# Kernel tuning notes

Hardware: AMD Instinct MI355X
Metric: run time of the kernel (lower is better)

## Reference

```python
import jax, jax.numpy as jnp
import numpy as np

D_MODEL = 1024
NUM_HEADS = 16
D_K = D_MODEL // NUM_HEADS


def setup_inputs() -> dict:
    key = jax.random.key(0)
    ks = jax.random.split(key, 9)
    B, S = 4, 2048
    s = 1.0 / np.sqrt(D_MODEL)
    inp = {
        "x": jax.random.normal(ks[0], (B, S, D_MODEL), dtype=jnp.float32),
        "wq": jax.random.uniform(ks[1], (D_MODEL, D_MODEL), jnp.float32, -s, s),
        "bq": jax.random.uniform(ks[2], (D_MODEL,), jnp.float32, -s, s),
        "wk": jax.random.uniform(ks[3], (D_MODEL, D_MODEL), jnp.float32, -s, s),
        "bk": jax.random.uniform(ks[4], (D_MODEL,), jnp.float32, -s, s),
        "wv": jax.random.uniform(ks[5], (D_MODEL, D_MODEL), jnp.float32, -s, s),
        "bv": jax.random.uniform(ks[6], (D_MODEL,), jnp.float32, -s, s),
        "wo": jax.random.uniform(ks[7], (D_MODEL, D_MODEL), jnp.float32, -s, s),
        "bo": jax.random.uniform(ks[8], (D_MODEL,), jnp.float32, -s, s),
    }
    return inp


def reference(x, wq, bq, wk, bk, wv, bv, wo, bo):
    B, S, _ = x.shape
    H, Dk = NUM_HEADS, D_K
    # QKV projections; weights stored as (in, out) so y = x @ w + b
    q = (x @ wq + bq).reshape(B, S, H, Dk).transpose(0, 2, 1, 3)  # (B,H,S,Dk)
    k = (x @ wk + bk).reshape(B, S, H, Dk).transpose(0, 2, 1, 3)
    v = (x @ wv + bv).reshape(B, S, H, Dk).transpose(0, 2, 1, 3)
    scores = jnp.einsum("bhqd,bhkd->bhqk", q, k) / jnp.sqrt(jnp.float32(Dk))
    causal = jnp.tril(jnp.ones((S, S), dtype=bool))  # True = keep
    scores = jnp.where(causal, scores, jnp.float32(-jnp.inf))
    attn = jax.nn.softmax(scores, axis=-1)  # dropout=0 (eval)
    out = jnp.einsum("bhqk,bhkd->bhqd", attn, v)
    out = out.transpose(0, 2, 1, 3).reshape(B, S, H * Dk)
    return out @ wo + bo
```

## Files before the change

kernel.cpp:

```cpp
#include <hip/hip_runtime.h>
#include <hip/hip_bf16.h>


#define D_MODEL 1024
#define NHEADS  16
#define DK      64
#define BATCH   4
#define SEQ     2048
#define MROWS   (BATCH*SEQ)

typedef short bvec8 __attribute__((ext_vector_type(8)));
typedef float fvec4  __attribute__((ext_vector_type(4)));
typedef float fvec16 __attribute__((ext_vector_type(16)));

__device__ __forceinline__ unsigned short f2bf(float f) {
    unsigned int x = __float_as_uint(f);
    x += 0x7fffu + ((x >> 16) & 1u);
    return (unsigned short)(x >> 16);
}
__device__ __forceinline__ float bf2f(unsigned short u) {
    return __uint_as_float(((unsigned int)u) << 16);
}

__device__ __forceinline__ unsigned pack_bf16x2(float a, float b) {
#if __has_builtin(__builtin_amdgcn_cvt_pk_bf16_f32)
    typedef __bf16 bf16x2_t __attribute__((ext_vector_type(2)));
    union { bf16x2_t v; unsigned u; } cv;
    cv.v = __builtin_amdgcn_cvt_pk_bf16_f32(a, b);
    return cv.u;
#else
    return (unsigned)f2bf(a) | ((unsigned)f2bf(b) << 16);
#endif
}

__device__ __forceinline__ float fast_exp2(float x) {
#if __has_builtin(__builtin_amdgcn_exp2f)
    return __builtin_amdgcn_exp2f(x);
#else
    return exp2f(x);
#endif
}


__global__ void f32_to_bf16_k(const float* __restrict__ in,
                              unsigned short* __restrict__ out, int n4) {
    int i = blockIdx.x * 256 + threadIdx.x;
    if (i < n4) {
        float4 v = ((const float4*)in)[i];
        ushort4 o;
        o.x = f2bf(v.x); o.y = f2bf(v.y); o.z = f2bf(v.z); o.w = f2bf(v.w);
        ((ushort4*)out)[i] = o;
    }
}

__global__ void transpose_all_k(const float* __restrict__ wq, const float* __restrict__ wk,
                                const float* __restrict__ wv, const float* __restrict__ wo,
                                unsigned short* __restrict__ wqkvt,
                                unsigned short* __restrict__ wot) {
    __shared__ float tile[32][33];
    const int z = blockIdx.z;
    const float* W = (z == 0) ? wq : (z == 1) ? wk : (z == 2) ? wv : wo;
    unsigned short* Wt = (z == 3) ? wot : wqkvt + (size_t)z * D_MODEL * D_MODEL;
    int n0 = blockIdx.x * 32, k0 = blockIdx.y * 32;
    int tx = threadIdx.x & 31;
    int ty = (threadIdx.x >> 5) * 4;
#pragma unroll
    for (int i = 0; i < 4; ++i)
        tile[ty + i][tx] = W[(k0 + ty + i) * D_MODEL + n0 + tx];
    __syncthreads();
#pragma unroll
    for (int i = 0; i < 4; ++i)
        Wt[(n0 + ty + i) * D_MODEL + k0 + tx] = f2bf(tile[tx][ty + i]);
}

__global__ void build_cbias_k(const float* __restrict__ bq, const float* __restrict__ bk,
                              const float* __restrict__ bv, float* __restrict__ cb) {
    int i = blockIdx.x * 256 + threadIdx.x;
    float v = (i < 1024) ? bq[i] : (i < 2048) ? bk[i - 1024] : bv[i - 2048];
    cb[i] = v;
}

__global__ __launch_bounds__(256, 2)
void gemm_glds(const unsigned short* __restrict__ A,
               const unsigned short* __restrict__ Bt,
               const float* __restrict__ bias,
               unsigned short* __restrict__ oq,
               unsigned short* __restrict__ ok,
               unsigned short* __restrict__ ov,
               float* __restrict__ of,
               float qscale, int mode) {
    __shared__ __align__(16) unsigned short As[2][128 * 64];
    __shared__ __align__(16) unsigned short Bs[2][128 * 64];

    const int tid  = threadIdx.x;
    const int lane = tid & 63;
    const int w    = tid >> 6;
    const int wr   = w >> 1, wc = w & 1;
    const int quad = lane >> 4, l16 = lane & 15;
    const int rowBlock = blockIdx.y * 128;
    const int colBlock = blockIdx.x * 128;

    const int lrow   = lane >> 3;
    const int gchunk = (lane & 7) ^ lrow;

    fvec4 acc[4][4] = {};

    {
#pragma unroll
        for (int n = 0; n < 4; ++n) {
            const int g = w * 4 + n;
            __builtin_amdgcn_global_load_lds(
                (const __attribute__((address_space(1))) void*)
                    &A[(size_t)(rowBlock + g * 8 + lrow) * D_MODEL + gchunk * 8],
                (__attribute__((address_space(3))) void*)&As[0][g * 512], 16, 0, 0);
            __builtin_amdgcn_global_load_lds(
                (const __attribute__((address_space(1))) void*)
                    &Bt[(size_t)(colBlock + g * 8 + lrow) * D_MODEL + gchunk * 8],
                (__attribute__((address_space(3))) void*)&Bs[0][g * 512], 16, 0, 0);
        }
    }

    for (int i = 0; i < 16; ++i) {
        __syncthreads();
        const int buf = i & 1;
        if (i < 15) {
            const int k1 = (i + 1) * 64;
#pragma unroll
            for (int n = 0; n < 4; ++n) {
                const int g = w * 4 + n;
                __builtin_amdgcn_global_load_lds(
                    (const __attribute__((address_space(1))) void*)
                        &A[(size_t)(rowBlock + g * 8 + lrow) * D_MODEL + k1 + gchunk * 8],
                    (__attribute__((address_space(3))) void*)&As[buf ^ 1][g * 512], 16, 0, 0);
                __builtin_amdgcn_global_load_lds(
                    (const __attribute__((address_space(1))) void*)
                        &Bt[(size_t)(colBlock + g * 8 + lrow) * D_MODEL + k1 + gchunk * 8],
                    (__attribute__((address_space(3))) void*)&Bs[buf ^ 1][g * 512], 16, 0, 0);
            }
        }
#pragma unroll
        for (int kc = 0; kc < 2; ++kc) {
            bvec8 af[4], bfr[4];
#pragma unroll
            for (int ii = 0; ii < 4; ++ii) {
                int r = wr * 64 + ii * 16 + l16;
                af[ii] = *(const bvec8*)&As[buf][r * 64 + (((kc * 4 + quad) ^ (l16 & 7)) * 8)];
            }
#pragma unroll
            for (int j = 0; j < 4; ++j) {
                int r = wc * 64 + j * 16 + l16;
                bfr[j] = *(const bvec8*)&Bs[buf][r * 64 + (((kc * 4 + quad) ^ (l16 & 7)) * 8)];
            }
#pragma unroll
            for (int ii = 0; ii < 4; ++ii)
#pragma unroll
                for (int j = 0; j < 4; ++j)
                    acc[ii][j] = __builtin_amdgcn_mfma_f32_16x16x32_bf16(
                        af[ii], bfr[j], acc[ii][j], 0, 0, 0);
        }
    }

    if (mode == 0) {
#pragma unroll
        for (int i = 0; i < 4; ++i) {
#pragma unroll
            for (int j = 0; j < 4; ++j) {
                int ncol = colBlock + wc * 64 + j * 16 + l16;
                int which = ncol >> 10;
                int nn = ncol & 1023;
                int h = nn >> 6, d = nn & 63;
                float bv = bias[ncol];
#pragma unroll
                for (int r = 0; r < 4; ++r) {
                    int mrow = rowBlock + wr * 64 + i * 16 + quad * 4 + r;
                    int b = mrow >> 11, s = mrow & (SEQ - 1);
                    float v = acc[i][j][r] + bv;
                    if (which == 0)
                        oq[(((b * NHEADS + h) * SEQ + s) * DK) + d] = f2bf(v * qscale);
                    else if (which == 1)
                        ok[(((b * NHEADS + h) * SEQ + s) * DK) + d] = f2bf(v);
                    else
                        ov[(((b * NHEADS + h) * DK + d) * SEQ) + s] = f2bf(v);
                }
            }
        }
    } else {
#pragma unroll
        for (int i = 0; i < 4; ++i) {
#pragma unroll
            for (int j = 0; j < 4; ++j) {
                int ncol = colBlock + wc * 64 + j * 16 + l16;
                float bv = bias[ncol];
#pragma unroll
                for (int r = 0; r < 4; ++r) {
                    int mrow = rowBlock + wr * 64 + i * 16 + quad * 4 + r;
                    of[(size_t)mrow * D_MODEL + ncol] = acc[i][j][r] + bv;
                }
            }
        }
    }
}

__global__ __launch_bounds__(256, 4)
void attn_mfmaA(const unsigned short* __restrict__ Q,
                const unsigned short* __restrict__ K,
                const unsigned short* __restrict__ Vt,
                unsigned short* __restrict__ O,
                unsigned short* __restrict__ Opart,
                float* __restrict__ Lpart) {
    __shared__ __align__(16) unsigned short Ksm[2][64 * 64];
    __shared__ __align__(16) unsigned short Vsm[2][64 * 64];
    __shared__ float Lsh[4][32];

    const int tid  = threadIdx.x;
    const int lane = tid & 63;
    const int wq   = tid >> 6;
    const int hf   = lane >> 5;
    const int l32  = lane & 31;
    const int hh = blockIdx.y, b = blockIdx.z;
    const int hb = b * NHEADS + hh;

    static const int qt_tbl[24] = {15,15,7,14,14,6,13,13,12,12,5,11,
                                   11,10,10,4,9,9,8,8,3,2,1,0};
    static const int md_tbl[24] = {0,1,2,0,1,2,0,1,0,1,2,0,
                                   1,0,1,2,0,1,0,1,2,2,2,2};
    const int bx = blockIdx.x;
    const int qt = qt_tbl[bx];
    const int md = md_tbl[bx];
    const bool part = (md < 2);
    const int kt0 = (md == 1) ? qt + 1 : 0;
    const int kt1 = (md == 0) ? qt + 1 : 2 * qt + 2;
    const int slot = part ? ((qt - 8) * 2 + md) : 0;

    const size_t bhq = ((size_t)hb) * SEQ * DK;
    const unsigned short* Qb = Q + bhq;
    const unsigned short* Kb = K + bhq;
    const unsigned short* Vb = Vt + bhq;

    const int q0 = qt * 128 + wq * 32;

    bvec8 qf[4];
#pragma unroll
    for (int kc = 0; kc < 4; ++kc)
        qf[kc] = *(const bvec8*)&Qb[(q0 + l32) * DK + kc * 16 + hf * 8];

    const int r1 = tid >> 3;
    const int lcs = (tid & 7) ^ (r1 & 7);

#define ATTN_STAGE(KT, NB) do {                                               \
    const unsigned short* kg_ = Kb + ((KT) * 64 + r1) * DK + lcs * 8;         \
    const unsigned short* vg_ = Vb + (size_t)r1 * SEQ + (KT) * 64 + lcs * 8;  \
    __builtin_amdgcn_global_load_lds(                                         \
        (const __attribute__((address_space(1))) void*)kg_,                   \
        (__attribute__((address_space(3))) void*)&Ksm[NB][wq * 512], 16, 0, 0); \
    __builtin_amdgcn_global_load_lds(                                         \
        (const __attribute__((address_space(1))) void*)(kg_ + 32 * DK),       \
        (__attribute__((address_space(3))) void*)&Ksm[NB][2048 + wq * 512], 16, 0, 0); \
    __builtin_amdgcn_global_load_lds(                                         \
        (const __attribute__((address_space(1))) void*)vg_,                   \
        (__attribute__((address_space(3))) void*)&Vsm[NB][wq * 512], 16, 0, 0); \
    __builtin_amdgcn_global_load_lds(                                         \
        (const __attribute__((address_space(1))) void*)(vg_ + 32 * SEQ),      \
        (__attribute__((address_space(3))) void*)&Vsm[NB][2048 + wq * 512], 16, 0, 0); \
} while (0)

    const int ktact = 2 * qt + (wq >> 1);
    const int mofs  = (wq & 1) << 5;

    ATTN_STAGE(kt0, 0);

    fvec16 acc0 = {};
    fvec16 acc1 = {};
    float lp = 0.f;

    for (int kt = kt0; kt < kt1; ++kt) {
        __syncthreads();
        const int buf = (kt - kt0) & 1;
        if (kt + 1 < kt1)
            ATTN_STAGE(kt + 1, buf ^ 1);
        if (kt <= ktact) {
            const unsigned short* Kbuf = &Ksm[buf][0];
            const unsigned short* Vbuf = &Vsm[buf][0];

            fvec16 s0 = {}, s1 = {};
            __builtin_amdgcn_s_setprio(1);
#pragma unroll
            for (int kc = 0; kc < 4; ++kc) {
                const int ch = (((kc * 2 + hf) ^ (l32 & 7)) * 8);
                bvec8 a0 = *(const bvec8*)&Kbuf[l32 * 64 + ch];
                bvec8 a1 = *(const bvec8*)&Kbuf[(32 + l32) * 64 + ch];
                s0 = __builtin_amdgcn_mfma_f32_32x32x16_bf16(a0, qf[kc], s0, 0, 0, 0);
                s1 = __builtin_amdgcn_mfma_f32_32x32x16_bf16(a1, qf[kc], s1, 0, 0, 0);
            }
            __builtin_amdgcn_s_setprio(0);

            if (kt == ktact) {
#pragma unroll
                for (int r = 0; r < 16; ++r) {
                    const int key0 = (r & 3) + 8 * (r >> 2) + 4 * hf - mofs;
                    if (key0 > l32)      s0[r] = -__builtin_inff();
                    if (key0 + 32 > l32) s1[r] = -__builtin_inff();
                }
            }

            unsigned pk[16];
#pragma unroll
            for (int m = 0; m < 8; ++m) {
                float p0 = fast_exp2(s0[2 * m]);
                float p1 = fast_exp2(s0[2 * m + 1]);
                float p2 = fast_exp2(s1[2 * m]);
                float p3 = fast_exp2(s1[2 * m + 1]);
                lp += (p0 + p1) + (p2 + p3);
                pk[m]     = pack_bf16x2(p0, p1);
                pk[8 + m] = pack_bf16x2(p2, p3);
            }

            __builtin_amdgcn_s_setprio(1);
#pragma unroll
            for (int kc16 = 0; kc16 < 4; ++kc16) {
                const int b0 = (kc16 >> 1) * 8 + (kc16 & 1) * 4;
                unsigned sw0 = __shfl_xor(pk[b0 + 0], 32);
                unsigned sw1 = __shfl_xor(pk[b0 + 1], 32);
                unsigned sw2 = __shfl_xor(pk[b0 + 2], 32);
                unsigned sw3 = __shfl_xor(pk[b0 + 3], 32);
                union { unsigned u[4]; bvec8 v; } afu;
                afu.u[0] = hf ? sw2 : pk[b0 + 0];
                afu.u[1] = hf ? sw3 : pk[b0 + 1];
                afu.u[2] = hf ? pk[b0 + 2] : sw0;
                afu.u[3] = hf ? pk[b0 + 3] : sw1;
                const int ch = (((kc16 * 2 + hf) ^ (l32 & 7)) * 8);
                bvec8 bv0 = *(const bvec8*)&Vbuf[l32 * 64 + ch];
                bvec8 bv1 = *(const bvec8*)&Vbuf[(32 + l32) * 64 + ch];
                acc0 = __builtin_amdgcn_mfma_f32_32x32x16_bf16(afu.v, bv0, acc0, 0, 0, 0);
                acc1 = __builtin_amdgcn_mfma_f32_32x32x16_bf16(afu.v, bv1, acc1, 0, 0, 0);
            }
            __builtin_amdgcn_s_setprio(0);
        }
    }
#undef ATTN_STAGE

    const float l = lp + __shfl_xor(lp, 32);

    if (part) {
        if (lane < 32)
            Lpart[((size_t)slot * 64 + hb) * 128 + wq * 32 + l32] = l;
        unsigned short* Od = Opart + (((size_t)slot * 64 + hb) * 128 + wq * 32) * 64;
#pragma unroll
        for (int g = 0; g < 4; ++g)
#pragma unroll
            for (int rr = 0; rr < 4; ++rr) {
                const int reg = g * 4 + rr;
                const int qrl = g * 8 + 4 * hf + rr;
                Od[(size_t)qrl * 64 + l32]      = f2bf(acc0[reg]);
                Od[(size_t)qrl * 64 + 32 + l32] = f2bf(acc1[reg]);
            }
    } else {
        if (lane < 32) Lsh[wq][l32] = l;
#pragma unroll
        for (int g = 0; g < 4; ++g) {
            float4 lv = *(const float4*)&Lsh[wq][g * 8 + 4 * hf];
#pragma unroll
            for (int rr = 0; rr < 4; ++rr) {
                const int reg = g * 4 + rr;
                const int qrow = q0 + g * 8 + 4 * hf + rr;
                const float inv = 1.f / ((const float*)&lv)[rr];
                unsigned short* dst = O + (size_t)(b * SEQ + qrow) * D_MODEL + hh * DK + l32;
                dst[0]  = f2bf(acc0[reg] * inv);
                dst[32] = f2bf(acc1[reg] * inv);
            }
        }
    }
}

__global__ void attn_combine_k(const unsigned short* __restrict__ Opart,
                               const float* __restrict__ Lpart,
                               unsigned short* __restrict__ O) {
    const int qt = 8 + blockIdx.x;
    const int h = blockIdx.y, b = blockIdx.z;
    const int hb = b * NHEADS + h;
    const int s0 = (qt - 8) * 2;
    const unsigned short* A  = Opart + ((size_t)(s0)*64 + hb) * 128 * 64;
    const unsigned short* Bp = Opart + ((size_t)(s0 + 1) * 64 + hb) * 128 * 64;
    const float* LA = Lpart + ((size_t)(s0)*64 + hb) * 128;
    const float* LB = Lpart + ((size_t)(s0 + 1) * 64 + hb) * 128;
    for (int e = threadIdx.x; e < 128 * 64; e += 256) {
        const int qr = e >> 6, d = e & 63;
        const float inv = 1.f / (LA[qr] + LB[qr]);
        const float v = (bf2f(A[e]) + bf2f(Bp[e])) * inv;
        O[(size_t)(b * SEQ + qt * 128 + qr) * D_MODEL + h * DK + d] = f2bf(v);
    }
}


extern "C" void kernel_launch(void* const* d_in, const int* in_sizes, int n_in,
                              void* d_out, int out_size, void* d_ws, size_t ws_size,
                              hipStream_t stream) {
    const float* x  = (const float*)d_in[0];
    const float* wq = (const float*)d_in[1];
    const float* bq = (const float*)d_in[2];
    const float* wk = (const float*)d_in[3];
    const float* bk = (const float*)d_in[4];
    const float* wv = (const float*)d_in[5];
    const float* bv = (const float*)d_in[6];
    const float* wo = (const float*)d_in[7];
    const float* bo = (const float*)d_in[8];
    float* out = (float*)d_out;

    char* ws = (char*)d_ws;
    const size_t MB = 1u << 20;
    unsigned short* xb    = (unsigned short*)(ws);
    unsigned short* wqkvt = (unsigned short*)(ws + 16 * MB);
    unsigned short* wot   = (unsigned short*)(ws + 22 * MB);
    unsigned short* qb    = (unsigned short*)(ws + 24 * MB);
    unsigned short* kb    = (unsigned short*)(ws + 40 * MB);
    unsigned short* vtb   = (unsigned short*)(ws + 56 * MB);
    unsigned short* ab    = (unsigned short*)(ws + 72 * MB);
    float* cbias = (float*)(ws + 72 * MB);
    unsigned short* Opart = (unsigned short*)(ws);
    float* Lpart = (float*)(ws + 16 * MB);

    f32_to_bf16_k<<<(MROWS * D_MODEL / 4 + 255) / 256, 256, 0, stream>>>(
        x, xb, MROWS * D_MODEL / 4);
    transpose_all_k<<<dim3(32, 32, 4), 256, 0, stream>>>(wq, wk, wv, wo, wqkvt, wot);
    build_cbias_k<<<12, 256, 0, stream>>>(bq, bk, bv, cbias);

    const float QSCALE = 0.125f * 1.44269504088896340736f;

    gemm_glds<<<dim3(3072 / 128, MROWS / 128), 256, 0, stream>>>(
        xb, wqkvt, cbias, qb, kb, vtb, nullptr, QSCALE, 0);

    attn_mfmaA<<<dim3(24, NHEADS, BATCH), 256, 0, stream>>>(
        qb, kb, vtb, ab, Opart, Lpart);
    attn_combine_k<<<dim3(8, NHEADS, BATCH), 256, 0, stream>>>(Opart, Lpart, ab);

    gemm_glds<<<dim3(D_MODEL / 128, MROWS / 128), 256, 0, stream>>>(
        ab, wot, bo, nullptr, nullptr, nullptr, out, 1.0f, 1);
}
```

Baseline: 296.9 us.

## Remap workgroups across XCDs and use permlane32_swap for P fragment exchange

Remaps the GEMM and attention block indices so consecutive work lands on the same XCD (f&7 stride mapping), aiming for better L2 locality of shared A/B tiles and K/V per head. In attention, replaces four ds_bpermute-based shfl_xor plus selects with two permlane32_swap instructions when the builtin is available, cutting LDS-path shuffle cost in the softmax-to-PV step. The remapping assumes grid sizes are divisible by 8 and changes the attention block order, which may affect the intended load-balancing of the qt table.

```diff
diff --git a/kernel.cpp b/kernel.cpp
--- a/kernel.cpp
+++ b/kernel.cpp
@@ -97,8 +97,12 @@
     const int w    = tid >> 6;
     const int wr   = w >> 1, wc = w & 1;
     const int quad = lane >> 4, l16 = lane & 15;
-    const int rowBlock = blockIdx.y * 128;
-    const int colBlock = blockIdx.x * 128;
+
+    const unsigned nwg = gridDim.x * gridDim.y;
+    unsigned f = blockIdx.y * gridDim.x + blockIdx.x;
+    f = (f & 7) * (nwg >> 3) + (f >> 3);
+    const int rowBlock = (f / gridDim.x) * 128;
+    const int colBlock = (f % gridDim.x) * 128;
 
     const int lrow   = lane >> 3;
     const int gchunk = (lane & 7) ^ lrow;
@@ -217,14 +221,18 @@
     const int wq   = tid >> 6;
     const int hf   = lane >> 5;
     const int l32  = lane & 31;
-    const int hh = blockIdx.y, b = blockIdx.z;
+
+    unsigned f = (blockIdx.z * 16 + blockIdx.y) * 24 + blockIdx.x;
+    f = (f & 7) * 192 + (f >> 3);
+    const int bx = f % 24;
+    const int hh = (f / 24) & 15;
+    const int b  = f / 384;
     const int hb = b * NHEADS + hh;
 
     static const int qt_tbl[24] = {15,15,7,14,14,6,13,13,12,12,5,11,
                                    11,10,10,4,9,9,8,8,3,2,1,0};
     static const int md_tbl[24] = {0,1,2,0,1,2,0,1,0,1,2,0,
                                    1,0,1,2,0,1,0,1,2,2,2,2};
-    const int bx = blockIdx.x;
     const int qt = qt_tbl[bx];
     const int md = md_tbl[bx];
     const bool part = (md < 2);
@@ -319,15 +327,31 @@
 #pragma unroll
             for (int kc16 = 0; kc16 < 4; ++kc16) {
                 const int b0 = (kc16 >> 1) * 8 + (kc16 & 1) * 4;
-                unsigned sw0 = __shfl_xor(pk[b0 + 0], 32);
-                unsigned sw1 = __shfl_xor(pk[b0 + 1], 32);
-                unsigned sw2 = __shfl_xor(pk[b0 + 2], 32);
-                unsigned sw3 = __shfl_xor(pk[b0 + 3], 32);
                 union { unsigned u[4]; bvec8 v; } afu;
-                afu.u[0] = hf ? sw2 : pk[b0 + 0];
-                afu.u[1] = hf ? sw3 : pk[b0 + 1];
-                afu.u[2] = hf ? pk[b0 + 2] : sw0;
-                afu.u[3] = hf ? pk[b0 + 3] : sw1;
+#if __has_builtin(__builtin_amdgcn_permlane32_swap)
+                {
+                    auto r02 = __builtin_amdgcn_permlane32_swap(
+                        pk[b0 + 0], pk[b0 + 2], false, false);
+                    auto r13 = __builtin_amdgcn_permlane32_swap(
+                        pk[b0 + 1], pk[b0 + 3], false, false);
+                    unsigned o02[2], o13[2];
+                    __builtin_memcpy(o02, &r02, 8);
+                    __builtin_memcpy(o13, &r13, 8);
+                    afu.u[0] = o02[0]; afu.u[2] = o02[1];
+                    afu.u[1] = o13[0]; afu.u[3] = o13[1];
+                }
+#else
+                {
+                    unsigned sw0 = __shfl_xor(pk[b0 + 0], 32);
+                    unsigned sw1 = __shfl_xor(pk[b0 + 1], 32);
+                    unsigned sw2 = __shfl_xor(pk[b0 + 2], 32);
+                    unsigned sw3 = __shfl_xor(pk[b0 + 3], 32);
+                    afu.u[0] = hf ? sw2 : pk[b0 + 0];
+                    afu.u[1] = hf ? sw3 : pk[b0 + 1];
+                    afu.u[2] = hf ? pk[b0 + 2] : sw0;
+                    afu.u[3] = hf ? pk[b0 + 3] : sw1;
+                }
+#endif
                 const int ch = (((kc16 * 2 + hf) ^ (l32 & 7)) * 8);
                 bvec8 bv0 = *(const bvec8*)&Vbuf[l32 * 64 + ch];
                 bvec8 bv1 = *(const bvec8*)&Vbuf[(32 + l32) * 64 + ch];
```

Result: faster. 284.6 us (-4.2%).
